# Kernel optimization log

Measured on AMD Instinct MI355X. Metric: run time of the kernel, lower is better.

## Reference

```python
import jax, jax.numpy as jnp
import numpy as np

B, L = 8, 1024
VOCAB, D_ENC, D_MAIN = 260, 128, 256
N_ENC, N_MAIN, N_DEC, N_HEADS = 3, 6, 3, 4
N_RATIO = 6.0  # 1/target_ratio
NEG = jnp.float32(-1e9)


def setup_inputs() -> dict:
    key = jax.random.key(0)
    kc = iter(jax.random.split(key, 40))
    def nrm(shape, std):
        return jax.random.normal(next(kc), shape, jnp.float32) * std
    inp = {'byte_ids': jax.random.randint(next(kc), (B, L), 0, VOCAB)}
    inp['embed'] = nrm((VOCAB, D_ENC), D_ENC ** -0.5)
    eye = jnp.eye(D_ENC, dtype=jnp.float32)
    inp['wq'] = eye + nrm((D_ENC, D_ENC), 0.02)  # init is identity in the torch module
    inp['wk'] = eye + nrm((D_ENC, D_ENC), 0.02)
    inp['proj_up'] = nrm((D_MAIN, D_ENC), D_ENC ** -0.5)
    inp['proj_down'] = nrm((D_ENC, D_MAIN), 1e-3)
    inp['norm_w'] = jnp.ones((D_ENC,), jnp.float32)
    inp['norm_b'] = jnp.zeros((D_ENC,), jnp.float32)
    for pre, n, d in [('enc', N_ENC, D_ENC), ('main', N_MAIN, D_MAIN), ('dec', N_DEC, D_ENC)]:
        inp[pre + '_ln1_w'] = jnp.ones((n, d), jnp.float32)
        inp[pre + '_ln1_b'] = jnp.zeros((n, d), jnp.float32)
        inp[pre + '_qkv'] = nrm((n, 3 * d, d), d ** -0.5)   # MHA in_proj (3D, D)
        inp[pre + '_wo'] = nrm((n, d, d), d ** -0.5)        # MHA out_proj
        inp[pre + '_ln2_w'] = jnp.ones((n, d), jnp.float32)
        inp[pre + '_ln2_b'] = jnp.zeros((n, d), jnp.float32)
        inp[pre + '_w1'] = nrm((n, 2 * d, d), d ** -0.5)    # mlp_mult = 2
        inp[pre + '_w2'] = nrm((n, d, 2 * d), (2 * d) ** -0.5)
    return inp


def _ln(x, w, b):
    mu = jnp.mean(x, axis=-1, keepdims=True)
    var = jnp.mean((x - mu) ** 2, axis=-1, keepdims=True)
    return (x - mu) * jax.lax.rsqrt(var + 1e-5) * w + b


def _mha(x, wqkv, wo, bias):
    Bb, S, D = x.shape
    dh = D // N_HEADS
    q, k, v = jnp.split(x @ wqkv.T, 3, axis=-1)
    q = q.reshape(Bb, S, N_HEADS, dh)
    k = k.reshape(Bb, S, N_HEADS, dh)
    v = v.reshape(Bb, S, N_HEADS, dh)
    scores = jnp.einsum('bqhd,bkhd->bhqk', q, k) * (dh ** -0.5) + bias
    attn = jax.nn.softmax(scores, axis=-1)
    out = jnp.einsum('bhqk,bkhd->bqhd', attn, v).reshape(Bb, S, D)
    return out @ wo.T


def _block(x, stack, i, bias):
    ln1w, ln1b, qkv, wo, ln2w, ln2b, w1, w2 = (a[i] for a in stack)
    x = x + _mha(_ln(x, ln1w, ln1b), qkv, wo, bias)
    h = _ln(x, ln2w, ln2b)
    return x + jax.nn.gelu(h @ w1.T, approximate=False) @ w2.T


def _downsample(x, b_hard):
    # scatter boundary tokens to the front of a padded (B, S, D) buffer
    Bb, S, D = x.shape
    idx = jnp.cumsum(b_hard, axis=1).astype(jnp.int32) - 1
    dest = jnp.where(b_hard > 0.5, idx, S)  # S is out-of-range -> dropped
    def sc(xb, db):
        return jnp.zeros((S, D), xb.dtype).at[db].set(xb, mode='drop')
    out = jax.vmap(sc)(x, dest)
    counts = jnp.sum(b_hard, axis=1).astype(jnp.int32)
    mask = jnp.arange(S)[None, :] < counts[:, None]
    return out, mask


def _forward(byte_ids, embed, wq, wk,
             enc_ln1_w, enc_ln1_b, enc_qkv, enc_wo, enc_ln2_w, enc_ln2_b, enc_w1, enc_w2,
             proj_up,
             main_ln1_w, main_ln1_b, main_qkv, main_wo, main_ln2_w, main_ln2_b, main_w1, main_w2,
             proj_down,
             dec_ln1_w, dec_ln1_b, dec_qkv, dec_wo, dec_ln2_w, dec_ln2_b, dec_w1, dec_w2,
             norm_w, norm_b):
    causal = jnp.where(jnp.triu(jnp.ones((L, L), bool), 1), NEG, jnp.float32(0.0))[None, None]
    x = embed[byte_ids]  # (B, L, D_ENC)
    enc_p = (enc_ln1_w, enc_ln1_b, enc_qkv, enc_wo, enc_ln2_w, enc_ln2_b, enc_w1, enc_w2)
    for i in range(N_ENC):
        x = _block(x, enc_p, i, causal)

    # --- dynamic chunking (routing + ratio loss) ---
    def l2n(t):
        return t / jnp.maximum(jnp.linalg.norm(t, axis=-1, keepdims=True), 1e-12)
    q = l2n(x @ wq.T)
    k = l2n(x @ wk.T)
    k_prev = jnp.pad(k[:, :-1], ((0, 0), (1, 0), (0, 0)))
    cos = jnp.sum(q * k_prev, axis=-1)
    p = jnp.clip(0.5 * (1.0 - cos), 0.0, 1.0)
    p = jnp.concatenate([jnp.ones_like(p[:, :1]), p[:, 1:]], axis=1)
    b_hard = (p >= 0.5).astype(jnp.float32)
    N = N_RATIO
    F_act = jnp.mean(b_hard)
    G_act = jnp.mean(p)
    ratio_loss = N / (N - 1.0) * ((N - 1.0) * F_act * G_act + (1.0 - F_act) * (1.0 - G_act))
    compressed, comp_mask = _downsample(x, b_hard)
    p_comp = _downsample(p[..., None], b_hard)[0][..., 0]

    # --- main stack on compressed sequence (padded to L, masked) ---
    z = compressed @ proj_up.T
    main_bias = causal + jnp.where(comp_mask, jnp.float32(0.0), NEG)[:, None, None, :]
    main_p = (main_ln1_w, main_ln1_b, main_qkv, main_wo, main_ln2_w, main_ln2_b, main_w1, main_w2)
    for i in range(N_MAIN):
        z = _block(z, main_p, i, main_bias)
    z = z @ proj_down.T  # (B, L, D_ENC)

    # --- chunk-level EMA (parallel linear-recurrence scan) + gather + STE ---
    p_c = jnp.clip(p_comp, 1e-4, 1.0 - 1e-4)
    a = (1.0 - p_c).at[:, 0].set(0.0)[..., None]          # z_bar[0] = z[0]
    bv = (p_c[..., None] * z).at[:, :1].set(z[:, :1])
    def comb(lhs, rhs):
        al, bl = lhs
        ar, br = rhs
        return (al * ar, ar * bl + br)
    z_bar = jax.lax.associative_scan(comb, (a, bv), axis=1)[1]
    chunk_idx = jnp.clip(jnp.cumsum(b_hard, axis=1).astype(jnp.int32) - 1, 0, None)
    z_up = jnp.take_along_axis(z_bar, jnp.broadcast_to(chunk_idx[:, :, None], z_bar.shape), axis=1)
    c = b_hard * p + (1.0 - b_hard) * (1.0 - p)
    c_ste = c + jax.lax.stop_gradient(1.0 - c)
    x = x + c_ste[..., None] * z_up

    dec_p = (dec_ln1_w, dec_ln1_b, dec_qkv, dec_wo, dec_ln2_w, dec_ln2_b, dec_w1, dec_w2)
    for i in range(N_DEC):
        x = _block(x, dec_p, i, causal)
    x = _ln(x, norm_w, norm_b)
    logits = x @ embed.T  # tied head
    return logits, ratio_loss


def reference(byte_ids, embed, wq, wk,
              enc_ln1_w, enc_ln1_b, enc_qkv, enc_wo, enc_ln2_w, enc_ln2_b, enc_w1, enc_w2,
              proj_up,
              main_ln1_w, main_ln1_b, main_qkv, main_wo, main_ln2_w, main_ln2_b, main_w1, main_w2,
              proj_down,
              dec_ln1_w, dec_ln1_b, dec_qkv, dec_wo, dec_ln2_w, dec_ln2_b, dec_w1, dec_w2,
              norm_w, norm_b):
    return _forward(byte_ids, embed, wq, wk,
                    enc_ln1_w, enc_ln1_b, enc_qkv, enc_wo, enc_ln2_w, enc_ln2_b, enc_w1, enc_w2,
                    proj_up,
                    main_ln1_w, main_ln1_b, main_qkv, main_wo, main_ln2_w, main_ln2_b, main_w1, main_w2,
                    proj_down,
                    dec_ln1_w, dec_ln1_b, dec_qkv, dec_wo, dec_ln2_w, dec_ln2_b, dec_w1, dec_w2,
                    norm_w, norm_b)
```

## Files before the change

kernel.cpp:

```cpp
#include <hip/hip_runtime.h>
#include <hip/hip_bf16.h>

#define B_ 8
#define L_ 1024
#define BL (B_*L_)
#define DENC 128
#define DMAIN 256
#define VOCAB 260
#define NHEADS 4

typedef __hip_bfloat16 bf16;
typedef _Float16 f16;
typedef f16 half8 __attribute__((ext_vector_type(8)));
typedef f16 half4 __attribute__((ext_vector_type(4)));
typedef f16 half2v __attribute__((ext_vector_type(2)));
typedef float f32x4 __attribute__((ext_vector_type(4)));

__global__ __launch_bounds__(64) void k_detect(const void* __restrict__ emb, int* __restrict__ flag){
    int lane = threadIdx.x;
    const unsigned short* u = (const unsigned short*)emb;
    int bad = 0;
    #pragma unroll
    for (int j = 0; j < 4; j++){
        unsigned short h = u[lane + 64*j];
        bf16 t = *(const bf16*)&h;
        float v = __bfloat162float(t);
        if (!(fabsf(v) < 1e4f)) bad++;
    }
    #pragma unroll
    for (int o = 32; o >= 1; o >>= 1) bad += __shfl_xor(bad, o);
    if (lane == 0) flag[0] = (bad == 0) ? 1 : 0;
}

struct CvtArgs {
    const void* src[31];
    unsigned offs[32];
};
__global__ void k_cvt_all(CvtArgs a, float* __restrict__ dst, f16* __restrict__ dst16,
                          int total, const int* __restrict__ flag, unsigned f32mask){
    int isbf = flag[0];
    for (int i = blockIdx.x*256 + threadIdx.x; i < total; i += gridDim.x*256){
        int lo = 0, hi = 30;
        while (lo < hi){ int mid = (lo+hi+1)>>1; if (a.offs[mid] <= (unsigned)i) lo = mid; else hi = mid-1; }
        int j = i - (int)a.offs[lo];
        float v = isbf ? __bfloat162float(((const bf16*)a.src[lo])[j])
                       : ((const float*)a.src[lo])[j];
        if ((f32mask >> lo) & 1u) dst[i] = v;
        dst16[i] = (f16)v;
    }
}

__global__ void k_embed(const int* __restrict__ ids, const float* __restrict__ emb, float* __restrict__ x){
    int i = blockIdx.x*256 + threadIdx.x;
    int row = i >> 7, d = i & 127;
    x[i] = emb[ids[row]*DENC + d];
}

template<int D>
__global__ __launch_bounds__(256) void k_ln16(const float* __restrict__ x, const float* __restrict__ w,
                                              const float* __restrict__ b, f16* __restrict__ y){
    int row = blockIdx.x*4 + (threadIdx.x >> 6);
    int lane = threadIdx.x & 63;
    const float* xr = x + (size_t)row*D;
    float v[D/64];
    float s = 0.f;
    #pragma unroll
    for (int j=0;j<D/64;j++){ v[j] = xr[lane + j*64]; s += v[j]; }
    #pragma unroll
    for (int o=32;o>=1;o>>=1) s += __shfl_xor(s,o);
    float mu = s / (float)D;
    float s2 = 0.f;
    #pragma unroll
    for (int j=0;j<D/64;j++){ float dd = v[j]-mu; s2 += dd*dd; }
    #pragma unroll
    for (int o=32;o>=1;o>>=1) s2 += __shfl_xor(s2,o);
    float inv = rsqrtf(s2/(float)D + 1e-5f);
    f16* yr = y + (size_t)row*D;
    #pragma unroll
    for (int j=0;j<D/64;j++){
        int d = lane + j*64;
        yr[d] = (f16)((v[j]-mu)*inv*w[d] + b[d]);
    }
}

#define GBM 64
#define GBN 64
#define GBK 32
__global__ __launch_bounds__(256) void k_gemm2(const float* __restrict__ A, const float* __restrict__ Wq,
        const float* __restrict__ Wk, float* __restrict__ Cq, float* __restrict__ Ck, int K)
{
    __shared__ float As[GBK][GBM+4];
    __shared__ float Ws[GBK][GBN+4];
    int tid = threadIdx.x;
    int bm = blockIdx.y * GBM;
    int bn = blockIdx.x * GBN;
    int tx = tid & 15, ty = tid >> 4;
    float acc[4][4] = {};
    for (int k0 = 0; k0 < K; k0 += GBK){
        #pragma unroll
        for (int i = tid; i < GBM*GBK; i += 256){
            int m = i >> 5, kk = i & 31;
            As[kk][m] = A[(size_t)(bm+m)*K + k0 + kk];
        }
        #pragma unroll
        for (int i = tid; i < GBN*GBK; i += 256){
            int n = i >> 5, kk = i & 31;
            int gn = bn + n;
            const float* W = (gn < 128) ? Wq : Wk;
            int wr = gn & 127;
            Ws[kk][n] = W[(size_t)wr*K + k0 + kk];
        }
        __syncthreads();
        #pragma unroll
        for (int kk = 0; kk < GBK; kk++){
            float a0[4], w0[4];
            *(float4*)a0 = *(const float4*)&As[kk][ty*4];
            *(float4*)w0 = *(const float4*)&Ws[kk][tx*4];
            #pragma unroll
            for (int i=0;i<4;i++)
                #pragma unroll
                for (int j=0;j<4;j++) acc[i][j] += a0[i]*w0[j];
        }
        __syncthreads();
    }
    #pragma unroll
    for (int i=0;i<4;i++){
        int m = bm + ty*4 + i;
        #pragma unroll
        for (int j=0;j<4;j++){
            int n = bn + tx*4 + j;
            float* C = (n < 128) ? Cq : Ck;
            C[(size_t)m*128 + (n & 127)] = acc[i][j];
        }
    }
}

template<int K>
__global__ __launch_bounds__(256) void k_hgemm(const f16* __restrict__ A, const f16* __restrict__ W,
        const float* __restrict__ R, float* __restrict__ C, f16* __restrict__ C16,
        void* __restrict__ OutRaw, const int* __restrict__ flag, int N, int mode,
        f16* __restrict__ Qd, f16* __restrict__ Kd, f16* __restrict__ Vd,
        int dShift, int dhShift)
{
    __shared__ half8 As[4][64];
    __shared__ half8 Ws[4][64];
    int tid = threadIdx.x;
    int wave = tid >> 6, lane = tid & 63;
    int wr = wave >> 1, wc = wave & 1;
    int quad = lane >> 4, l15 = lane & 15;
    int bm = blockIdx.y * 64, bn = blockIdx.x * 64;

    f32x4 acc[2][2] = {};
    int srow = tid >> 2, sc8 = tid & 3;
    const f16* ap0 = A + (size_t)(bm + srow)*K + sc8*8;
    int gn = bn + srow;
    const f16* wp0 = W + (size_t)gn*K + sc8*8;
    bool wok = (gn < N);

    for (int k0 = 0; k0 < K; k0 += 32){
        __syncthreads();
        As[sc8][srow] = *(const half8*)(ap0 + k0);
        Ws[sc8][srow] = wok ? *(const half8*)(wp0 + k0) : (half8)(f16)0.f;
        __syncthreads();
        half8 af[2], wf[2];
        af[0] = As[quad][wr*32 + l15];
        af[1] = As[quad][wr*32 + 16 + l15];
        wf[0] = Ws[quad][wc*32 + l15];
        wf[1] = Ws[quad][wc*32 + 16 + l15];
        #pragma unroll
        for (int i=0;i<2;i++)
            #pragma unroll
            for (int j=0;j<2;j++)
                acc[i][j] = __builtin_amdgcn_mfma_f32_16x16x32_f16(af[i], wf[j], acc[i][j], 0, 0, 0);
    }

    #pragma unroll
    for (int j=0;j<2;j++){
        int n = bn + wc*32 + j*16 + l15;
        if (n >= N) continue;
        #pragma unroll
        for (int i=0;i<2;i++){
            #pragma unroll
            for (int r=0;r<4;r++){
                int m = bm + wr*32 + i*16 + quad*4 + r;
                float v = acc[i][j][r];
                if (mode == 5){
                    int which = n >> dShift;
                    int rem = n & ((1<<dShift)-1);
                    int hh = rem >> dhShift;
                    int dd = rem & ((1<<dhShift)-1);
                    int bb = m >> 10, tt = m & 1023;
                    int Hn = 1 << (dShift - dhShift);
                    f16* dst = (which==0) ? Qd : ((which==1) ? Kd : Vd);
                    if (which == 2)
                        dst[((((size_t)bb*Hn + hh) << dhShift) + dd)*L_ + tt] = (f16)v;
                    else
                        dst[((((size_t)bb*Hn + hh)*L_ + tt) << dhShift) + dd] = (f16)v;
                    continue;
                }
                size_t off = (size_t)m*N + n;
                if (mode == 1){ C[off] = v + R[off]; }
                else if (mode == 2){
                    v = 0.5f*v*(1.0f + erff(v*0.70710678118654752f));
                    C16[off] = (f16)v;
                } else if (mode == 3){
                    if (flag[0]) ((bf16*)OutRaw)[off] = __float2bfloat16(v);
                    else         ((float*)OutRaw)[off] = v;
                } else C[off] = v;
            }
        }
    }
}

template<int K>
__global__ __launch_bounds__(256) void k_lngemm(const float* __restrict__ A, const f16* __restrict__ W,
        const float* __restrict__ lnw, const float* __restrict__ lnb, int doLN,
        float* __restrict__ C, void* __restrict__ OutRaw,
        const int* __restrict__ flag, int N, int mode)
{
    constexpr int SA = K + 8;
    constexpr int RPT = K/64;
    __shared__ f16 sA[64*SA];
    int tid = threadIdx.x;
    int wave = tid >> 6, lane = tid & 63;
    int wr = wave >> 1, wc = wave & 1;
    int quad = lane >> 4, l15 = lane & 15;
    int bm = blockIdx.y * 64, bn = blockIdx.x * 64;

    float wv_[RPT], bv_[RPT];
    #pragma unroll
    for (int j=0;j<RPT;j++){
        int d = lane*RPT + j;
        wv_[j] = doLN ? lnw[d] : 1.f;
        bv_[j] = doLN ? lnb[d] : 0.f;
    }
    for (int rr=0; rr<16; rr++){
        int row = wave*16 + rr;
        const float* xr = A + (size_t)(bm+row)*K + lane*RPT;
        float v[RPT];
        if (RPT==2){ float2 t = *(const float2*)xr; v[0]=t.x; v[1]=t.y; }
        else       { float4 t = *(const float4*)xr; v[0]=t.x; v[1]=t.y; v[2]=t.z; v[3]=t.w; }
        float mu = 0.f, inv = 1.f;
        if (doLN){
            float s=0.f;
            #pragma unroll
            for (int j=0;j<RPT;j++) s += v[j];
            #pragma unroll
            for (int o=32;o>=1;o>>=1) s += __shfl_xor(s,o);
            mu = s / (float)K;
            float s2=0.f;
            #pragma unroll
            for (int j=0;j<RPT;j++){ float dd=v[j]-mu; s2+=dd*dd; }
            #pragma unroll
            for (int o=32;o>=1;o>>=1) s2 += __shfl_xor(s2,o);
            inv = rsqrtf(s2/(float)K + 1e-5f);
        }
        if (RPT==2){
            half2v h;
            h[0]=(f16)((v[0]-mu)*inv*wv_[0]+bv_[0]);
            h[1]=(f16)((v[1]-mu)*inv*wv_[1]+bv_[1]);
            *(half2v*)&sA[row*SA + lane*2] = h;
        } else {
            half4 h;
            #pragma unroll
            for (int j=0;j<4;j++) h[j]=(f16)((v[j]-mu)*inv*wv_[j]+bv_[j]);
            *(half4*)&sA[row*SA + lane*4] = h;
        }
    }
    __syncthreads();

    f32x4 acc[2][2] = {};
    int n0 = bn + wc*32 + l15;
    bool ok0 = n0 < N, ok1 = (n0+16) < N;
    const f16* w0p = W + (size_t)n0*K + quad*8;
    const f16* w1p = W + (size_t)(n0+16)*K + quad*8;
    #pragma unroll 4
    for (int k0=0;k0<K;k0+=32){
        half8 af[2], wf[2];
        af[0] = *(const half8*)&sA[(wr*32 + l15)*SA + k0 + quad*8];
        af[1] = *(const half8*)&sA[(wr*32 + 16 + l15)*SA + k0 + quad*8];
        wf[0] = ok0 ? *(const half8*)(w0p + k0) : (half8)(f16)0.f;
        wf[1] = ok1 ? *(const half8*)(w1p + k0) : (half8)(f16)0.f;
        #pragma unroll
        for (int i=0;i<2;i++)
            #pragma unroll
            for (int j=0;j<2;j++)
                acc[i][j] = __builtin_amdgcn_mfma_f32_16x16x32_f16(af[i], wf[j], acc[i][j], 0, 0, 0);
    }

    #pragma unroll
    for (int j=0;j<2;j++){
        int n = bn + wc*32 + j*16 + l15;
        if (n >= N) continue;
        #pragma unroll
        for (int i=0;i<2;i++){
            #pragma unroll
            for (int r=0;r<4;r++){
                int m = bm + wr*32 + i*16 + quad*4 + r;
                float v = acc[i][j][r];
                size_t off = (size_t)m*N + n;
                if (mode == 3){
                    if (flag[0]) ((bf16*)OutRaw)[off] = __float2bfloat16(v);
                    else         ((float*)OutRaw)[off] = v;
                } else C[off] = v;
            }
        }
    }
}

template<int DH>
__global__ __launch_bounds__(256) void k_mflash(const f16* __restrict__ Qh, const f16* __restrict__ Kh,
        const f16* __restrict__ Vt, f16* __restrict__ out, const int* __restrict__ counts,
        float scale)
{
    constexpr int BQ = 64, BK = 64;
    constexpr int RS = DH + 8;
    constexpr int PS = BK + 8;
    __shared__ f16 sQ[BQ*RS];
    __shared__ f16 sK[BK*RS];
    __shared__ f16 sVt[DH*PS];
    __shared__ f16 sP[BQ*PS];

    int x = blockIdx.x, b = x >> 2, h = x & 3;
    int yy = blockIdx.y;
    int qt = (yy < 8) ? yy : 23 - yy;
    int q0 = qt * BQ;
    int tid = threadIdx.x;
    int wv = tid >> 6, lane = tid & 63;
    int quad = lane >> 4, l15 = lane & 15;

    const f16* Qb = Qh + (size_t)x*L_*DH;
    const f16* Kb = Kh + (size_t)x*L_*DH;
    const f16* Vb = Vt + (size_t)x*DH*L_;
    int kcap = counts ? counts[b] : L_;
    int klen = min(kcap, q0 + BQ);

    for (int i = tid; i < BQ*DH/8; i += 256){
        int r = (8*i)/DH, c = (8*i)%DH;
        *(half8*)&sQ[r*RS + c] = *(const half8*)&Qb[(size_t)(q0+r)*DH + c];
    }

    float m[4], l[4];
    #pragma unroll
    for (int r=0;r<4;r++){ m[r] = -1e30f; l[r] = 0.f; }
    f32x4 accO[DH/16] = {};

    for (int k0 = 0; k0 < klen; k0 += BK){
        __syncthreads();
        for (int i = tid; i < BK*DH/8; i += 256){
            int r = (8*i)/DH, c = (8*i)%DH;
            *(half8*)&sK[r*RS + c] = *(const half8*)&Kb[(size_t)(k0+r)*DH + c];
        }
        for (int i = tid; i < DH*BK/8; i += 256){
            int r = (8*i)/BK, c = (8*i)%BK;
            *(half8*)&sVt[r*PS + c] = *(const half8*)&Vb[(size_t)r*L_ + k0 + c];
        }
        __syncthreads();

        half8 af[DH/32];
        #pragma unroll
        for (int ds=0; ds<DH/32; ds++)
            af[ds] = *(const half8*)&sQ[(16*wv + l15)*RS + quad*8 + 32*ds];
        f32x4 accS[4] = {};
        #pragma unroll
        for (int t=0;t<4;t++){
            #pragma unroll
            for (int ds=0; ds<DH/32; ds++){
                half8 bf = *(const half8*)&sK[(16*t + l15)*RS + quad*8 + 32*ds];
                accS[t] = __builtin_amdgcn_mfma_f32_16x16x32_f16(af[ds], bf, accS[t], 0, 0, 0);
            }
        }

        #pragma unroll
        for (int r=0;r<4;r++){
            int qrow = q0 + 16*wv + quad*4 + r;
            float sv[4];
            #pragma unroll
            for (int t=0;t<4;t++){
                float v = accS[t][r]*scale;
                int kp = k0 + 16*t + l15;
                if (kp > qrow || kp >= kcap) v = -1e30f;
                sv[t] = v;
            }
            float rm = fmaxf(fmaxf(sv[0],sv[1]), fmaxf(sv[2],sv[3]));
            rm = fmaxf(rm, __shfl_xor(rm, 1));
            rm = fmaxf(rm, __shfl_xor(rm, 2));
            rm = fmaxf(rm, __shfl_xor(rm, 4));
            rm = fmaxf(rm, __shfl_xor(rm, 8));
            float mn = fmaxf(m[r], rm);
            float al = __expf(m[r] - mn);
            float p0 = __expf(sv[0]-mn), p1 = __expf(sv[1]-mn);
            float p2 = __expf(sv[2]-mn), p3 = __expf(sv[3]-mn);
            float rs = p0+p1+p2+p3;
            rs += __shfl_xor(rs, 1);
            rs += __shfl_xor(rs, 2);
            rs += __shfl_xor(rs, 4);
            rs += __shfl_xor(rs, 8);
            l[r] = l[r]*al + rs;
            m[r] = mn;
            #pragma unroll
            for (int dt=0; dt<DH/16; dt++) accO[dt][r] *= al;
            int prow = 16*wv + quad*4 + r;
            sP[prow*PS + 16*0 + l15] = (f16)p0;
            sP[prow*PS + 16*1 + l15] = (f16)p1;
            sP[prow*PS + 16*2 + l15] = (f16)p2;
            sP[prow*PS + 16*3 + l15] = (f16)p3;
        }

        half8 pf[2];
        #pragma unroll
        for (int ks=0; ks<2; ks++)
            pf[ks] = *(const half8*)&sP[(16*wv + l15)*PS + quad*8 + 32*ks];
        #pragma unroll
        for (int dt=0; dt<DH/16; dt++){
            #pragma unroll
            for (int ks=0; ks<2; ks++){
                half8 bv = *(const half8*)&sVt[(16*dt + l15)*PS + quad*8 + 32*ks];
                accO[dt] = __builtin_amdgcn_mfma_f32_16x16x32_f16(pf[ks], bv, accO[dt], 0, 0, 0);
            }
        }
    }

    #pragma unroll
    for (int r=0;r<4;r++){
        float inv = 1.0f / l[r];
        int qrow = q0 + 16*wv + quad*4 + r;
        #pragma unroll
        for (int dt=0; dt<DH/16; dt++){
            int d = 16*dt + l15;
            out[((size_t)b*L_ + qrow)*(NHEADS*DH) + h*DH + d] = (f16)(accO[dt][r]*inv);
        }
    }
}

__global__ __launch_bounds__(64) void k_router(const float* __restrict__ Q, const float* __restrict__ Kr,
        float* __restrict__ p, float* __restrict__ bh, float* __restrict__ acc)
{
    int idx = blockIdx.x;
    int t = idx & (L_-1);
    int lane = threadIdx.x;
    if (idx == 0 && lane < 8) acc[lane] = 0.f;
    float pv;
    if (t == 0){ pv = 1.0f; }
    else {
        const float* qr = Q  + (size_t)idx*DENC;
        const float* kr = Kr + (size_t)(idx-1)*DENC;
        float qq=0.f, kk=0.f, qk=0.f;
        #pragma unroll
        for (int j=0;j<2;j++){
            float qv = qr[lane + j*64], kv = kr[lane + j*64];
            qq += qv*qv; kk += kv*kv; qk += qv*kv;
        }
        #pragma unroll
        for (int o=32;o>=1;o>>=1){ qq += __shfl_xor(qq,o); kk += __shfl_xor(kk,o); qk += __shfl_xor(qk,o); }
        float cosv = qk / (fmaxf(sqrtf(qq),1e-12f)*fmaxf(sqrtf(kk),1e-12f));
        pv = 0.5f*(1.0f - cosv);
        pv = fminf(fmaxf(pv, 0.0f), 1.0f);
    }
    if (lane == 0){ p[idx] = pv; bh[idx] = (pv >= 0.5f) ? 1.0f : 0.0f; }
}

__global__ __launch_bounds__(64) void k_seq(const float* __restrict__ bh, const float* __restrict__ p,
                      int* __restrict__ cidx, int* __restrict__ src, int* __restrict__ counts,
                      float* __restrict__ acc){
    int b = blockIdx.x;
    int lane = threadIdx.x;
    int base = b*L_ + lane*16;
    int h[16];
    int cnt = 0;
    float ps = 0.f;
    #pragma unroll
    for (int j=0;j<16;j++){ h[j] = bh[base+j] > 0.5f; cnt += h[j]; ps += p[base+j]; }
    int inc = cnt;
    #pragma unroll
    for (int o=1;o<64;o<<=1){ int nb = __shfl_up(inc, o); if (lane >= o) inc += nb; }
    int run = inc - cnt;
    #pragma unroll
    for (int j=0;j<16;j++){
        run += h[j];
        int ci = run - 1; if (ci < 0) ci = 0;
        cidx[base+j] = ci;
        if (h[j]) src[b*L_ + run-1] = lane*16 + j;
    }
    float cs = (float)cnt;
    #pragma unroll
    for (int o=32;o>=1;o>>=1){ ps += __shfl_xor(ps,o); cs += __shfl_xor(cs,o); }
    if (lane == 0){ atomicAdd(&acc[0], ps); atomicAdd(&acc[1], cs); }
    if (lane == 63) counts[b] = inc;
}

__global__ __launch_bounds__(128) void k_scatter2(const float* __restrict__ x, const float* __restrict__ p,
        const int* __restrict__ src, const int* __restrict__ counts,
        f16* __restrict__ comp, float* __restrict__ pcomp)
{
    int s = blockIdx.x & (L_-1), b = blockIdx.x >> 10, d = threadIdx.x;
    int cnt = counts[b];
    f16* crow = comp + ((size_t)b*L_ + s)*DENC;
    if (s < cnt){
        int t = src[b*L_ + s];
        crow[d] = (f16)x[((size_t)b*L_ + t)*DENC + d];
        if (d == 0) pcomp[b*L_ + s] = p[b*L_ + t];
    } else {
        crow[d] = (f16)0.f;
        if (d == 0) pcomp[b*L_ + s] = 0.f;
    }
}

__global__ __launch_bounds__(256) void k_ema2(const float* __restrict__ z, const float* __restrict__ pcomp,
                                              float* __restrict__ zbar){
    __shared__ float sp[L_];
    int blk = blockIdx.x;
    int b = blk >> 5;
    int tid = threadIdx.x, wv = tid >> 6, lane = tid & 63;
    int d = ((blk & 31) << 2) + wv;
    for (int i = tid; i < L_; i += 256){
        float pc = pcomp[b*L_ + i];
        sp[i] = fminf(fmaxf(pc, 1e-4f), 1.0f - 1e-4f);
    }
    __syncthreads();
    const float* zb = z + ((size_t)b*L_)*DENC + d;
    int t0 = lane*16;
    float zv[16];
    #pragma unroll
    for (int i=0;i<16;i++) zv[i] = zb[(size_t)(t0+i)*DENC];
    float A = 1.f, Bv = 0.f;
    #pragma unroll
    for (int i=0;i<16;i++){
        int t = t0 + i;
        float pc = sp[t];
        float a  = (t==0) ? 0.f : (1.f - pc);
        float bb = (t==0) ? zv[i] : pc*zv[i];
        A = a*A;
        Bv = a*Bv + bb;
    }
    #pragma unroll
    for (int off=1; off<64; off<<=1){
        float Ap = __shfl_up(A, off);
        float Bp = __shfl_up(Bv, off);
        if (lane >= off){ Bv = A*Bp + Bv; A = A*Ap; }
    }
    float sin_ = __shfl_up(Bv, 1);
    if (lane == 0) sin_ = 0.f;
    float s = sin_;
    float* ob = zbar + ((size_t)b*L_)*DENC + d;
    #pragma unroll
    for (int i=0;i<16;i++){
        int t = t0 + i;
        float pc = sp[t];
        float a  = (t==0) ? 0.f : (1.f - pc);
        float bb = (t==0) ? zv[i] : pc*zv[i];
        s = a*s + bb;
        ob[(size_t)t*DENC] = s;
    }
}

__global__ void k_combine(float* __restrict__ x, const float* __restrict__ zbar, const int* __restrict__ cidx){
    int i = blockIdx.x*256 + threadIdx.x;
    int row = i >> 7, d = i & 127;
    int b = row >> 10;
    int ci = cidx[row];
    x[i] += zbar[((size_t)b*L_ + ci)*DENC + d];
}

__global__ void k_loss(const float* __restrict__ acc, void* __restrict__ out, const int* __restrict__ flag){
    float G = acc[0] / (float)BL;
    float F = acc[1] / (float)BL;
    float ratio = 1.2f*(5.0f*F*G + (1.0f-F)*(1.0f-G));
    if (flag[0]) ((bf16*)out)[(size_t)BL*VOCAB] = __float2bfloat16(ratio);
    else         ((float*)out)[(size_t)BL*VOCAB] = ratio;
}

extern "C" void kernel_launch(void* const* d_in, const int* in_sizes, int n_in,
                              void* d_out, int out_size, void* d_ws, size_t ws_size,
                              hipStream_t stream) {
    (void)out_size; (void)ws_size;
    const int* byte_ids = (const int*)d_in[0];

    float* ws = (float*)d_ws;
    size_t off = 0;
    int* FLAG = (int*)ws; off += 16;
    float* W32 = ws + off;

    k_detect<<<1, 64, 0, stream>>>(d_in[1], FLAG);

    CvtArgs ca;
    const float* w32[32];
    unsigned woff = 0;
    for (int i = 1; i < n_in && i < 32; i++){
        w32[i] = W32 + woff;
        ca.src[i-1] = d_in[i];
        ca.offs[i-1] = woff;
        woff += (unsigned)in_sizes[i];
    }
    ca.offs[31] = woff;
    off += woff;
    f16* W16h = (f16*)(ws + off); off += (woff+1)/2;
    const f16* w16[32];
    for (int i = 1; i < n_in && i < 32; i++) w16[i] = W16h + ca.offs[i-1];
    k_cvt_all<<<2048, 256, 0, stream>>>(ca, W32, W16h, (int)woff, FLAG, 0x199999E7u);

    const float* embed    = w32[1];
    const float* wq       = w32[2];
    const float* wk       = w32[3];
    const float* norm_w   = w32[6];
    const float* norm_b   = w32[7];

    float* X    = ws + off; off += (size_t)BL*DENC;
    float* QKVf = ws + off; off += (size_t)BL*3*DMAIN;
    float* ATTf = ws + off; off += (size_t)BL*DMAIN;
    float* Hf   = ws + off; off += (size_t)BL*2*DMAIN;
    float* LNf  = ws + off; off += (size_t)BL*DMAIN;
    float* Z    = ws + off; off += (size_t)BL*DMAIN;
    float* COMPf= ws + off; off += (size_t)BL*DENC;
    float* P    = ws + off; off += BL;
    float* BH   = ws + off; off += BL;
    float* PCOMP= ws + off; off += BL;
    float* ACC  = ws + off; off += 8;
    int* CIDX   = (int*)(ws + off); off += BL;
    int* SRC    = (int*)(ws + off); off += BL;
    int* COUNTS = (int*)(ws + off); off += 64;

    f16* QKV16 = (f16*)QKVf;
    f16* ATT16 = (f16*)ATTf;
    f16* H16   = (f16*)Hf;
    f16* LN16  = (f16*)LNf;
    f16* COMP16= (f16*)COMPf;
    float* Qr  = ATTf;
    float* Kr  = Hf;
    float* ZDN = QKVf;
    float* ZBAR= QKVf + (size_t)BL*DENC;

    auto hgemm = [&](int K, const f16* A, const f16* W, const float* R, float* C, f16* C16,
                     void* Ob, int N, int mode, f16* Qd, f16* Kd, f16* Vd, int dS, int dhS){
        dim3 g((N+63)/64, BL/64);
        if (K == 128)      k_hgemm<128><<<g,256,0,stream>>>(A, W, R, C, C16, Ob, FLAG, N, mode, Qd, Kd, Vd, dS, dhS);
        else if (K == 256) k_hgemm<256><<<g,256,0,stream>>>(A, W, R, C, C16, Ob, FLAG, N, mode, Qd, Kd, Vd, dS, dhS);
        else               k_hgemm<512><<<g,256,0,stream>>>(A, W, R, C, C16, Ob, FLAG, N, mode, Qd, Kd, Vd, dS, dhS);
    };

    auto block128 = [&](float* Xs, const float* l1w, const float* l1b, const f16* qkvw, const f16* wo,
                        const float* l2w, const float* l2b, const f16* w1, const f16* w2){
        k_ln16<128><<<BL/4,256,0,stream>>>(Xs, l1w, l1b, LN16);
        hgemm(128, LN16, qkvw, nullptr, nullptr, nullptr, nullptr, 3*DENC, 5,
              QKV16, QKV16 + (size_t)BL*DENC, QKV16 + (size_t)2*BL*DENC, 7, 5);
        k_mflash<32><<<dim3(B_*NHEADS,16),256,0,stream>>>(QKV16, QKV16 + (size_t)BL*DENC,
                                                          QKV16 + (size_t)2*BL*DENC,
                                                          ATT16, nullptr, 0.17677669529663687f);
        hgemm(128, ATT16, wo, Xs, Xs, nullptr, nullptr, DENC, 1, nullptr, nullptr, nullptr, 0, 0);
        k_ln16<128><<<BL/4,256,0,stream>>>(Xs, l2w, l2b, LN16);
        hgemm(128, LN16, w1, nullptr, nullptr, H16, nullptr, 2*DENC, 2, nullptr, nullptr, nullptr, 0, 0);
        hgemm(256, H16, w2, Xs, Xs, nullptr, nullptr, DENC, 1, nullptr, nullptr, nullptr, 0, 0);
    };
    auto block_main = [&](float* Xs, const float* l1w, const float* l1b, const f16* qkvw, const f16* wo,
                          const float* l2w, const float* l2b, const f16* w1, const f16* w2){
        k_ln16<256><<<BL/4,256,0,stream>>>(Xs, l1w, l1b, LN16);
        hgemm(256, LN16, qkvw, nullptr, nullptr, nullptr, nullptr, 3*DMAIN, 5,
              QKV16, QKV16 + (size_t)BL*DMAIN, QKV16 + (size_t)2*BL*DMAIN, 8, 6);
        k_mflash<64><<<dim3(B_*NHEADS,16),256,0,stream>>>(QKV16, QKV16 + (size_t)BL*DMAIN,
                                                          QKV16 + (size_t)2*BL*DMAIN,
                                                          ATT16, COUNTS, 0.125f);
        hgemm(256, ATT16, wo, Xs, Xs, nullptr, nullptr, DMAIN, 1, nullptr, nullptr, nullptr, 0, 0);
        k_ln16<256><<<BL/4,256,0,stream>>>(Xs, l2w, l2b, LN16);
        hgemm(256, LN16, w1, nullptr, nullptr, H16, nullptr, 2*DMAIN, 2, nullptr, nullptr, nullptr, 0, 0);
        hgemm(512, H16, w2, Xs, Xs, nullptr, nullptr, DMAIN, 1, nullptr, nullptr, nullptr, 0, 0);
    };

    k_embed<<<BL*DENC/256, 256, 0, stream>>>(byte_ids, embed, X);
    for (int i = 0; i < 3; i++)
        block128(X, w32[8] + i*DENC, w32[9] + i*DENC, w16[10] + (size_t)i*3*DENC*DENC,
                 w16[11] + (size_t)i*DENC*DENC, w32[12] + i*DENC, w32[13] + i*DENC,
                 w16[14] + (size_t)i*2*DENC*DENC, w16[15] + (size_t)i*2*DENC*DENC);

    k_gemm2<<<dim3(4, BL/64), 256, 0, stream>>>(X, wq, wk, Qr, Kr, DENC);
    k_router<<<BL, 64, 0, stream>>>(Qr, Kr, P, BH, ACC);
    k_seq<<<B_, 64, 0, stream>>>(BH, P, CIDX, SRC, COUNTS, ACC);
    k_scatter2<<<BL, 128, 0, stream>>>(X, P, SRC, COUNTS, COMP16, PCOMP);

    hgemm(128, COMP16, w16[4], nullptr, Z, nullptr, nullptr, DMAIN, 0, nullptr, nullptr, nullptr, 0, 0);
    for (int i = 0; i < 6; i++)
        block_main(Z, w32[16] + i*DMAIN, w32[17] + i*DMAIN, w16[18] + (size_t)i*3*DMAIN*DMAIN,
                   w16[19] + (size_t)i*DMAIN*DMAIN, w32[20] + i*DMAIN, w32[21] + i*DMAIN,
                   w16[22] + (size_t)i*2*DMAIN*DMAIN, w16[23] + (size_t)i*2*DMAIN*DMAIN);
    k_lngemm<256><<<dim3(2, BL/64), 256, 0, stream>>>(Z, w16[5], nullptr, nullptr, 0,
                                                      ZDN, nullptr, FLAG, DENC, 0);

    k_ema2<<<256, 256, 0, stream>>>(ZDN, PCOMP, ZBAR);
    k_combine<<<BL*DENC/256, 256, 0, stream>>>(X, ZBAR, CIDX);

    for (int i = 0; i < 3; i++)
        block128(X, w32[24] + i*DENC, w32[25] + i*DENC, w16[26] + (size_t)i*3*DENC*DENC,
                 w16[27] + (size_t)i*DENC*DENC, w32[28] + i*DENC, w32[29] + i*DENC,
                 w16[30] + (size_t)i*2*DENC*DENC, w16[31] + (size_t)i*2*DENC*DENC);

    k_lngemm<128><<<dim3(5, BL/64), 256, 0, stream>>>(X, w16[1], norm_w, norm_b, 1,
                                                      nullptr, d_out, FLAG, VOCAB, 3);
    k_loss<<<1,1,0,stream>>>(ACC, d_out, FLAG);
}
```

Before: 1.242 ms.

## Fuse residual-add GEMM epilogues with following LayerNorm across all blocks

Adds a GEMM kernel whose 32-row tiles cover the full output width, so the residual add and the next LayerNorm (producing the fp16 normalized input) happen in the epilogue. Embedding lookup and decoder combine are also fused with the first LayerNorm. This removes the standalone LayerNorm launches and their extra passes over the activations. In exchange the new GEMM uses a single-block-row tile with no K-loop double buffering, which may lower GEMM efficiency, and the final head now reads the precomputed LN output.

After: 1.168 ms. -6.0%, faster.

```diff
diff --git a/kernel.cpp b/kernel.cpp
--- a/kernel.cpp
+++ b/kernel.cpp
@@ -50,10 +50,27 @@
     }
 }
 
-__global__ void k_embed(const int* __restrict__ ids, const float* __restrict__ emb, float* __restrict__ x){
-    int i = blockIdx.x*256 + threadIdx.x;
-    int row = i >> 7, d = i & 127;
-    x[i] = emb[ids[row]*DENC + d];
+__global__ __launch_bounds__(256) void k_embed_ln(const int* __restrict__ ids, const float* __restrict__ emb,
+        const float* __restrict__ lnw, const float* __restrict__ lnb,
+        float* __restrict__ x, f16* __restrict__ y){
+    int row = blockIdx.x*4 + (threadIdx.x >> 6);
+    int lane = threadIdx.x & 63;
+    int id = ids[row];
+    float v0 = emb[(size_t)id*DENC + lane];
+    float v1 = emb[(size_t)id*DENC + 64 + lane];
+    x[(size_t)row*DENC + lane] = v0;
+    x[(size_t)row*DENC + 64 + lane] = v1;
+    float s = v0 + v1;
+    #pragma unroll
+    for (int o=32;o>=1;o>>=1) s += __shfl_xor(s,o);
+    float mu = s / (float)DENC;
+    float d0 = v0-mu, d1 = v1-mu;
+    float s2 = d0*d0 + d1*d1;
+    #pragma unroll
+    for (int o=32;o>=1;o>>=1) s2 += __shfl_xor(s2,o);
+    float inv = rsqrtf(s2/(float)DENC + 1e-5f);
+    y[(size_t)row*DENC + lane]      = (f16)(d0*inv*lnw[lane] + lnb[lane]);
+    y[(size_t)row*DENC + 64 + lane] = (f16)(d1*inv*lnw[64+lane] + lnb[64+lane]);
 }
 
 template<int D>
@@ -212,6 +229,103 @@
     }
 }
 
+template<int K, int N>
+__global__ __launch_bounds__(256) void k_gfl(const f16* __restrict__ A, const f16* __restrict__ W,
+        const float* __restrict__ R, float* __restrict__ X, f16* __restrict__ Y,
+        const float* __restrict__ lnw, const float* __restrict__ lnb, int doLN, int hasR)
+{
+    constexpr int NT2 = N/32;
+    __shared__ half8 As[4][32];
+    __shared__ half8 Ws[4][N];
+    __shared__ float sred[2][2][32];
+    int tid = threadIdx.x;
+    int wave = tid >> 6, lane = tid & 63;
+    int wr = wave >> 1, wc = wave & 1;
+    int quad = lane >> 4, l15 = lane & 15;
+    int bm = blockIdx.x * 32;
+
+    f32x4 acc[NT2] = {};
+    int srow = (tid & 127) >> 2, sch = tid & 3;
+    const f16* ap0 = A + (size_t)(bm + srow)*K + sch*8;
+    int s4 = tid >> 2;
+
+    for (int k0 = 0; k0 < K; k0 += 32){
+        __syncthreads();
+        if (tid < 128) As[sch][srow] = *(const half8*)(ap0 + k0);
+        #pragma unroll
+        for (int s = 0; s < N/64; s++){
+            int rr = s4 + s*64;
+            Ws[sch][rr] = *(const half8*)(W + (size_t)rr*K + sch*8 + k0);
+        }
+        __syncthreads();
+        half8 af = As[quad][wr*16 + l15];
+        #pragma unroll
+        for (int j=0;j<NT2;j++){
+            half8 wf = Ws[quad][(wc*NT2 + j)*16 + l15];
+            acc[j] = __builtin_amdgcn_mfma_f32_16x16x32_f16(af, wf, acc[j], 0, 0, 0);
+        }
+    }
+
+    float v[NT2][4];
+    #pragma unroll
+    for (int r=0;r<4;r++){
+        int row = bm + wr*16 + quad*4 + r;
+        #pragma unroll
+        for (int j=0;j<NT2;j++){
+            int col = (wc*NT2 + j)*16 + l15;
+            float rv = hasR ? R[(size_t)row*N + col] : 0.f;
+            v[j][r] = acc[j][r] + rv;
+            X[(size_t)row*N + col] = v[j][r];
+        }
+    }
+    if (doLN){
+        int lrow0 = wr*16 + quad*4;
+        float mu[4], inv[4];
+        #pragma unroll
+        for (int r=0;r<4;r++){
+            float s = 0.f;
+            #pragma unroll
+            for (int j=0;j<NT2;j++) s += v[j][r];
+            s += __shfl_xor(s, 1); s += __shfl_xor(s, 2);
+            s += __shfl_xor(s, 4); s += __shfl_xor(s, 8);
+            if (l15 == 0) sred[0][wc][lrow0 + r] = s;
+        }
+        __syncthreads();
+        #pragma unroll
+        for (int r=0;r<4;r++)
+            mu[r] = (sred[0][0][lrow0 + r] + sred[0][1][lrow0 + r]) / (float)N;
+        #pragma unroll
+        for (int r=0;r<4;r++){
+            float s2 = 0.f;
+            #pragma unroll
+            for (int j=0;j<NT2;j++){ float dd = v[j][r] - mu[r]; s2 += dd*dd; }
+            s2 += __shfl_xor(s2, 1); s2 += __shfl_xor(s2, 2);
+            s2 += __shfl_xor(s2, 4); s2 += __shfl_xor(s2, 8);
+            if (l15 == 0) sred[1][wc][lrow0 + r] = s2;
+        }
+        __syncthreads();
+        #pragma unroll
+        for (int r=0;r<4;r++)
+            inv[r] = rsqrtf((sred[1][0][lrow0 + r] + sred[1][1][lrow0 + r]) / (float)N + 1e-5f);
+        float wv_[NT2], bv_[NT2];
+        #pragma unroll
+        for (int j=0;j<NT2;j++){
+            int col = (wc*NT2 + j)*16 + l15;
+            wv_[j] = lnw[col];
+            bv_[j] = lnb[col];
+        }
+        #pragma unroll
+        for (int r=0;r<4;r++){
+            int row = bm + wr*16 + quad*4 + r;
+            #pragma unroll
+            for (int j=0;j<NT2;j++){
+                int col = (wc*NT2 + j)*16 + l15;
+                Y[(size_t)row*N + col] = (f16)((v[j][r] - mu[r])*inv[r]*wv_[j] + bv_[j]);
+            }
+        }
+    }
+}
+
 template<int K>
 __global__ __launch_bounds__(256) void k_lngemm(const float* __restrict__ A, const f16* __restrict__ W,
         const float* __restrict__ lnw, const float* __restrict__ lnb, int doLN,
@@ -554,12 +668,29 @@
     }
 }
 
-__global__ void k_combine(float* __restrict__ x, const float* __restrict__ zbar, const int* __restrict__ cidx){
-    int i = blockIdx.x*256 + threadIdx.x;
-    int row = i >> 7, d = i & 127;
+__global__ __launch_bounds__(256) void k_combine_ln(float* __restrict__ x, const float* __restrict__ zbar,
+        const int* __restrict__ cidx, const float* __restrict__ lnw, const float* __restrict__ lnb,
+        f16* __restrict__ y){
+    int row = blockIdx.x*4 + (threadIdx.x >> 6);
+    int lane = threadIdx.x & 63;
     int b = row >> 10;
     int ci = cidx[row];
-    x[i] += zbar[((size_t)b*L_ + ci)*DENC + d];
+    const float* zr = zbar + ((size_t)b*L_ + ci)*DENC;
+    float v0 = x[(size_t)row*DENC + lane]      + zr[lane];
+    float v1 = x[(size_t)row*DENC + 64 + lane] + zr[64 + lane];
+    x[(size_t)row*DENC + lane] = v0;
+    x[(size_t)row*DENC + 64 + lane] = v1;
+    float s = v0 + v1;
+    #pragma unroll
+    for (int o=32;o>=1;o>>=1) s += __shfl_xor(s,o);
+    float mu = s / (float)DENC;
+    float d0 = v0-mu, d1 = v1-mu;
+    float s2 = d0*d0 + d1*d1;
+    #pragma unroll
+    for (int o=32;o>=1;o>>=1) s2 += __shfl_xor(s2,o);
+    float inv = rsqrtf(s2/(float)DENC + 1e-5f);
+    y[(size_t)row*DENC + lane]      = (f16)(d0*inv*lnw[lane] + lnb[lane]);
+    y[(size_t)row*DENC + 64 + lane] = (f16)(d1*inv*lnw[64+lane] + lnb[64+lane]);
 }
 
 __global__ void k_loss(const float* __restrict__ acc, void* __restrict__ out, const int* __restrict__ flag){
@@ -637,62 +768,75 @@
         else if (K == 256) k_hgemm<256><<<g,256,0,stream>>>(A, W, R, C, C16, Ob, FLAG, N, mode, Qd, Kd, Vd, dS, dhS);
         else               k_hgemm<512><<<g,256,0,stream>>>(A, W, R, C, C16, Ob, FLAG, N, mode, Qd, Kd, Vd, dS, dhS);
     };
-
-    auto block128 = [&](float* Xs, const float* l1w, const float* l1b, const f16* qkvw, const f16* wo,
-                        const float* l2w, const float* l2b, const f16* w1, const f16* w2){
-        k_ln16<128><<<BL/4,256,0,stream>>>(Xs, l1w, l1b, LN16);
+    auto gfl = [&](int K, int N, const f16* A, const f16* W, const float* R, float* Xo, f16* Y,
+                   const float* lw, const float* lb, int doLN, int hasR){
+        dim3 g(BL/32);
+        if (K == 128 && N == 128)      k_gfl<128,128><<<g,256,0,stream>>>(A, W, R, Xo, Y, lw, lb, doLN, hasR);
+        else if (K == 256 && N == 128) k_gfl<256,128><<<g,256,0,stream>>>(A, W, R, Xo, Y, lw, lb, doLN, hasR);
+        else if (K == 128 && N == 256) k_gfl<128,256><<<g,256,0,stream>>>(A, W, R, Xo, Y, lw, lb, doLN, hasR);
+        else if (K == 256 && N == 256) k_gfl<256,256><<<g,256,0,stream>>>(A, W, R, Xo, Y, lw, lb, doLN, hasR);
+        else                           k_gfl<512,256><<<g,256,0,stream>>>(A, W, R, Xo, Y, lw, lb, doLN, hasR);
+    };
+
+    auto block128 = [&](float* Xs, const f16* qkvw, const f16* wo,
+                        const float* l2w, const float* l2b, const f16* w1, const f16* w2,
+                        const float* nlw, const float* nlb, int doNext){
         hgemm(128, LN16, qkvw, nullptr, nullptr, nullptr, nullptr, 3*DENC, 5,
               QKV16, QKV16 + (size_t)BL*DENC, QKV16 + (size_t)2*BL*DENC, 7, 5);
         k_mflash<32><<<dim3(B_*NHEADS,16),256,0,stream>>>(QKV16, QKV16 + (size_t)BL*DENC,
                                                           QKV16 + (size_t)2*BL*DENC,
                                                           ATT16, nullptr, 0.17677669529663687f);
-        hgemm(128, ATT16, wo, Xs, Xs, nullptr, nullptr, DENC, 1, nullptr, nullptr, nullptr, 0, 0);
-        k_ln16<128><<<BL/4,256,0,stream>>>(Xs, l2w, l2b, LN16);
+        gfl(128, 128, ATT16, wo, Xs, Xs, LN16, l2w, l2b, 1, 1);
         hgemm(128, LN16, w1, nullptr, nullptr, H16, nullptr, 2*DENC, 2, nullptr, nullptr, nullptr, 0, 0);
-        hgemm(256, H16, w2, Xs, Xs, nullptr, nullptr, DENC, 1, nullptr, nullptr, nullptr, 0, 0);
+        gfl(256, 128, H16, w2, Xs, Xs, LN16, nlw, nlb, doNext, 1);
     };
-    auto block_main = [&](float* Xs, const float* l1w, const float* l1b, const f16* qkvw, const f16* wo,
-                          const float* l2w, const float* l2b, const f16* w1, const f16* w2){
-        k_ln16<256><<<BL/4,256,0,stream>>>(Xs, l1w, l1b, LN16);
+    auto block_main = [&](float* Xs, const f16* qkvw, const f16* wo,
+                          const float* l2w, const float* l2b, const f16* w1, const f16* w2,
+                          const float* nlw, const float* nlb, int doNext){
         hgemm(256, LN16, qkvw, nullptr, nullptr, nullptr, nullptr, 3*DMAIN, 5,
               QKV16, QKV16 + (size_t)BL*DMAIN, QKV16 + (size_t)2*BL*DMAIN, 8, 6);
         k_mflash<64><<<dim3(B_*NHEADS,16),256,0,stream>>>(QKV16, QKV16 + (size_t)BL*DMAIN,
                                                           QKV16 + (size_t)2*BL*DMAIN,
                                                           ATT16, COUNTS, 0.125f);
-        hgemm(256, ATT16, wo, Xs, Xs, nullptr, nullptr, DMAIN, 1, nullptr, nullptr, nullptr, 0, 0);
-        k_ln16<256><<<BL/4,256,0,stream>>>(Xs, l2w, l2b, LN16);
+        gfl(256, 256, ATT16, wo, Xs, Xs, LN16, l2w, l2b, 1, 1);
         hgemm(256, LN16, w1, nullptr, nullptr, H16, nullptr, 2*DMAIN, 2, nullptr, nullptr, nullptr, 0, 0);
-        hgemm(512, H16, w2, Xs, Xs, nullptr, nullptr, DMAIN, 1, nullptr, nullptr, nullptr, 0, 0);
+        gfl(512, 256, H16, w2, Xs, Xs, LN16, nlw, nlb, doNext, 1);
     };
 
-    k_embed<<<BL*DENC/256, 256, 0, stream>>>(byte_ids, embed, X);
+    k_embed_ln<<<BL/4, 256, 0, stream>>>(byte_ids, embed, w32[8], w32[9], X, LN16);
     for (int i = 0; i < 3; i++)
-        block128(X, w32[8] + i*DENC, w32[9] + i*DENC, w16[10] + (size_t)i*3*DENC*DENC,
-                 w16[11] + (size_t)i*DENC*DENC, w32[12] + i*DENC, w32[13] + i*DENC,
-                 w16[14] + (size_t)i*2*DENC*DENC, w16[15] + (size_t)i*2*DENC*DENC);
+        block128(X, w16[10] + (size_t)i*3*DENC*DENC, w16[11] + (size_t)i*DENC*DENC,
+                 w32[12] + i*DENC, w32[13] + i*DENC,
+                 w16[14] + (size_t)i*2*DENC*DENC, w16[15] + (size_t)i*2*DENC*DENC,
+                 (i < 2) ? w32[8] + (i+1)*DENC : nullptr,
+                 (i < 2) ? w32[9] + (i+1)*DENC : nullptr, (i < 2) ? 1 : 0);
 
     k_gemm2<<<dim3(4, BL/64), 256, 0, stream>>>(X, wq, wk, Qr, Kr, DENC);
     k_router<<<BL, 64, 0, stream>>>(Qr, Kr, P, BH, ACC);
     k_seq<<<B_, 64, 0, stream>>>(BH, P, CIDX, SRC, COUNTS, ACC);
     k_scatter2<<<BL, 128, 0, stream>>>(X, P, SRC, COUNTS, COMP16, PCOMP);
 
-    hgemm(128, COMP16, w16[4], nullptr, Z, nullptr, nullptr, DMAIN, 0, nullptr, nullptr, nullptr, 0, 0);
+    gfl(128, 256, COMP16, w16[4], nullptr, Z, LN16, w32[16], w32[17], 1, 0);
     for (int i = 0; i < 6; i++)
-        block_main(Z, w32[16] + i*DMAIN, w32[17] + i*DMAIN, w16[18] + (size_t)i*3*DMAIN*DMAIN,
-                   w16[19] + (size_t)i*DMAIN*DMAIN, w32[20] + i*DMAIN, w32[21] + i*DMAIN,
-                   w16[22] + (size_t)i*2*DMAIN*DMAIN, w16[23] + (size_t)i*2*DMAIN*DMAIN);
+        block_main(Z, w16[18] + (size_t)i*3*DMAIN*DMAIN, w16[19] + (size_t)i*DMAIN*DMAIN,
+                   w32[20] + i*DMAIN, w32[21] + i*DMAIN,
+                   w16[22] + (size_t)i*2*DMAIN*DMAIN, w16[23] + (size_t)i*2*DMAIN*DMAIN,
+                   (i < 5) ? w32[16] + (i+1)*DMAIN : nullptr,
+                   (i < 5) ? w32[17] + (i+1)*DMAIN : nullptr, (i < 5) ? 1 : 0);
     k_lngemm<256><<<dim3(2, BL/64), 256, 0, stream>>>(Z, w16[5], nullptr, nullptr, 0,
                                                       ZDN, nullptr, FLAG, DENC, 0);
 
     k_ema2<<<256, 256, 0, stream>>>(ZDN, PCOMP, ZBAR);
-    k_combine<<<BL*DENC/256, 256, 0, stream>>>(X, ZBAR, CIDX);
+    k_combine_ln<<<BL/4, 256, 0, stream>>>(X, ZBAR, CIDX, w32[24], w32[25], LN16);
 
     for (int i = 0; i < 3; i++)
-        block128(X, w32[24] + i*DENC, w32[25] + i*DENC, w16[26] + (size_t)i*3*DENC*DENC,
-                 w16[27] + (size_t)i*DENC*DENC, w32[28] + i*DENC, w32[29] + i*DENC,
-                 w16[30] + (size_t)i*2*DENC*DENC, w16[31] + (size_t)i*2*DENC*DENC);
-
-    k_lngemm<128><<<dim3(5, BL/64), 256, 0, stream>>>(X, w16[1], norm_w, norm_b, 1,
-                                                      nullptr, d_out, FLAG, VOCAB, 3);
+        block128(X, w16[26] + (size_t)i*3*DENC*DENC, w16[27] + (size_t)i*DENC*DENC,
+                 w32[28] + i*DENC, w32[29] + i*DENC,
+                 w16[30] + (size_t)i*2*DENC*DENC, w16[31] + (size_t)i*2*DENC*DENC,
+                 (i < 2) ? w32[24] + (i+1)*DENC : norm_w,
+                 (i < 2) ? w32[25] + (i+1)*DENC : norm_b, 1);
+
+    hgemm(128, LN16, w16[1], nullptr, nullptr, nullptr, d_out, VOCAB, 3,
+          nullptr, nullptr, nullptr, 0, 0);
     k_loss<<<1,1,0,stream>>>(ACC, d_out, FLAG);
 }
```
